# Performance work log

Measured on AMD Instinct MI355X. Metric: run time of the kernel, lower is better.

The kernel has to match this reference:

```python
import jax, jax.numpy as jnp
import numpy as np

B, N, M = 8, 1024, 1024
D_MODEL, D_HEAD, M_BITS = 1024, 128, 32
SCALE = 1.0 / np.sqrt(M_BITS)


def setup_inputs() -> dict:
    key = jax.random.key(0)
    ks = jax.random.split(key, 11)
    w_std = 1.0 / np.sqrt(D_MODEL)  # ~ nn.Linear init scale
    f32 = jnp.float32
    return {
        "Q": jax.random.normal(ks[0], (B, N, D_MODEL), dtype=f32),
        "K": jax.random.normal(ks[1], (B, M, D_MODEL), dtype=f32),
        "V": jax.random.normal(ks[2], (B, M, D_MODEL), dtype=f32),
        "Wq_boolean": jax.random.normal(ks[3], (D_MODEL, M_BITS), dtype=f32) * w_std,
        "Wk_boolean": jax.random.normal(ks[4], (D_MODEL, M_BITS), dtype=f32) * w_std,
        "Wq_tropical": jax.random.normal(ks[5], (D_MODEL, M_BITS), dtype=f32) * w_std,
        "Wk_tropical": jax.random.normal(ks[6], (D_MODEL, M_BITS), dtype=f32) * w_std,
        "Wq_real": jax.random.normal(ks[7], (D_MODEL, M_BITS), dtype=f32) * w_std,
        "Wk_real": jax.random.normal(ks[8], (D_MODEL, M_BITS), dtype=f32) * w_std,
        "Wv": jax.random.normal(ks[9], (D_MODEL, D_HEAD), dtype=f32) * w_std,
        "fusion_weights": jnp.ones((3,), dtype=f32),
        "mask": jnp.ones((B, N, M), dtype=jnp.int32),
    }


def _tropical_sim(Qe, Ke):
    # max-plus (tropical) witness similarity: sim[b,n,m] = max_d (Qe[b,n,d] + Ke[b,m,d])
    # loop over the small fixed bit dim (M_BITS=32) to avoid a [B,N,M,M_BITS] tensor
    acc = Qe[:, :, 0][:, :, None] + Ke[:, :, 0][:, None, :]
    for b in range(1, M_BITS):
        acc = jnp.maximum(acc, Qe[:, :, b][:, :, None] + Ke[:, :, b][:, None, :])
    return acc  # [B,N,M]


def reference(Q, K, V, Wq_boolean, Wk_boolean, Wq_tropical, Wk_tropical,
              Wq_real, Wk_real, Wv, fusion_weights, mask):
    # --- boolean monoid: hard-binarized codes, bit-match count ---
    Qb = (Q @ Wq_boolean > 0).astype(Q.dtype)   # [B,N,m]
    Kb = (K @ Wk_boolean > 0).astype(K.dtype)   # [B,M,m]
    sim_bool = (jnp.einsum('bnd,bmd->bnm', Qb, Kb)
                + jnp.einsum('bnd,bmd->bnm', 1.0 - Qb, 1.0 - Kb))
    # --- tropical monoid: max-plus over continuous codes ---
    sim_trop = _tropical_sim(Q @ Wq_tropical, K @ Wk_tropical)
    # --- real monoid: inner product of continuous codes ---
    sim_real = jnp.einsum('bnd,bmd->bnm', Q @ Wq_real, K @ Wk_real)
    # --- learned fusion + scaled softmax attention ---
    w = jax.nn.softmax(fusion_weights)
    scores = (w[0] * sim_bool + w[1] * sim_trop + w[2] * sim_real) * SCALE
    scores = jnp.where(mask == 0, -jnp.inf, scores)
    attn = jax.nn.softmax(scores, axis=-1)     # [B,N,M]  (dropout: eval mode, identity)
    out = jnp.einsum('bnm,bmh->bnh', attn, V @ Wv)  # [B,N,d_head]
    return out, attn
```

## Files before the change

kernel.cpp:

```cpp
#include <hip/hip_runtime.h>
#include <hip/hip_fp16.h>
#include <stdint.h>
#include <math.h>


#define SCALE_F 0.17677669529663687f

typedef float4 f4;
typedef unsigned int uint_t;
typedef unsigned short ushort_t;
typedef __attribute__((ext_vector_type(8))) short s16x8;
typedef __attribute__((ext_vector_type(8))) unsigned short u16x8;
typedef __attribute__((ext_vector_type(4))) float f32x4;

__device__ __forceinline__ ushort_t f2bf(float x) {
    unsigned u = __float_as_uint(x);
    return (ushort_t)((u + 0x7FFFu + ((u >> 16) & 1u)) >> 16);
}
__device__ __forceinline__ float bf2f(ushort_t h) {
    return __uint_as_float(((unsigned)h) << 16);
}
__device__ __forceinline__ float f4c(const f4 v, int i) {
    return i == 0 ? v.x : (i == 1 ? v.y : (i == 2 ? v.z : v.w));
}
__device__ __forceinline__ unsigned pk_add(unsigned a, unsigned b) {
    unsigned r;
    asm("v_pk_add_f16 %0, %1, %2" : "=v"(r) : "v"(a), "v"(b));
    return r;
}
__device__ __forceinline__ unsigned pk_max(unsigned a, unsigned b) {
    unsigned r;
    asm("v_pk_max_f16 %0, %1, %2" : "=v"(r) : "v"(a), "v"(b));
    return r;
}
__device__ __forceinline__ float h2f(ushort_t u) {
    __half h;
    *reinterpret_cast<ushort_t*>(&h) = u;
    return __half2float(h);
}
__device__ __forceinline__ ushort_t f2h(float x) {
    __half h = __float2half(x);
    return *reinterpret_cast<ushort_t*>(&h);
}

#define MFMA16(a, b, c) __builtin_amdgcn_mfma_f32_16x16x32_bf16((a), (b), (c), 0, 0, 0)

__device__ __forceinline__ int bo(int col, int kq) {
    return col * 64 + 8 * (kq ^ (col & 7));
}
__device__ __forceinline__ int fillk(int s) {
    return 8 * ((s & 7) ^ ((s >> 3) & 7));
}

__global__ __launch_bounds__(256)
void conv_w_kernel(const float* __restrict__ Wqb, const float* __restrict__ Wkb,
                   const float* __restrict__ Wqt, const float* __restrict__ Wkt,
                   const float* __restrict__ Wqr, const float* __restrict__ Wkr,
                   const float* __restrict__ Wv,
                   ushort_t* __restrict__ Wh, ushort_t* __restrict__ Wm,
                   ushort_t* __restrict__ Wl3,
                   ushort_t* __restrict__ Wvh, ushort_t* __restrict__ Wvm) {
    __shared__ float T[256][33];
    const int t = threadIdx.x;
    const int bid = blockIdx.x;
    const float* src;
    int kb, outRowBase, srcStride, srcColBase, side = 0;
    bool isQK, isBool;
    if (bid < 24) {
        side = bid / 12;
        int cb = (bid % 12) / 4;
        kb = bid & 3;
        const float* mats[6] = {Wqb, Wqt, Wqr, Wkb, Wkt, Wkr};
        src = mats[side * 3 + cb];
        srcStride = 32; srcColBase = 0;
        outRowBase = side * 96 + cb * 32;
        isQK = true; isBool = (cb == 0);
    } else {
        int v = bid - 24;
        int hb = v >> 2; kb = v & 3;
        src = Wv; srcStride = 128; srcColBase = hb * 32;
        outRowBase = hb * 32;
        isQK = false; isBool = false;
    }
    #pragma unroll
    for (int i = 0; i < 8; ++i) {
        int idx = t + i * 256;
        int r = idx >> 3, c4 = idx & 7;
        f4 v = *(const f4*)&src[(size_t)(kb * 256 + r) * srcStride + srcColBase + c4 * 4];
        T[r][c4 * 4 + 0] = v.x; T[r][c4 * 4 + 1] = v.y;
        T[r][c4 * 4 + 2] = v.z; T[r][c4 * 4 + 3] = v.w;
    }
    __syncthreads();
    const int col = t >> 3, kseg = t & 7;
    ushort_t* dh = isQK ? Wh : Wvh;
    ushort_t* dm = isQK ? Wm : Wvm;
    size_t obase = (size_t)(outRowBase + col) * 1024 + kb * 256 + kseg * 32;
    u16x8 ph[4], pm[4], pl[4];
    #pragma unroll
    for (int i = 0; i < 32; ++i) {
        float x = T[kseg * 32 + i][col];
        ushort_t hb_ = f2bf(x);
        float r1 = x - bf2f(hb_);
        ushort_t mb_ = f2bf(r1);
        float r2 = r1 - bf2f(mb_);
        ph[i >> 3][i & 7] = hb_;
        pm[i >> 3][i & 7] = mb_;
        pl[i >> 3][i & 7] = f2bf(r2);
    }
    #pragma unroll
    for (int i = 0; i < 4; ++i) {
        *(u16x8*)&dh[obase + i * 8] = ph[i];
        *(u16x8*)&dm[obase + i * 8] = pm[i];
    }
    if (isBool) {
        size_t lbase = (size_t)(side * 32 + col) * 1024 + kb * 256 + kseg * 32;
        #pragma unroll
        for (int i = 0; i < 4; ++i) *(u16x8*)&Wl3[lbase + i * 8] = pl[i];
    }
}


__global__ __launch_bounds__(256)
void proj_qk_kernel(const float* __restrict__ Q, const float* __restrict__ K,
                    const ushort_t* __restrict__ Wh, const ushort_t* __restrict__ Wm,
                    ushort_t* __restrict__ Qt_q, ushort_t* __restrict__ Kt_q,
                    ushort_t* __restrict__ Qrh, ushort_t* __restrict__ Qrm,
                    ushort_t* __restrict__ Krh, ushort_t* __restrict__ Krm,
                    uint_t* __restrict__ Qbits, uint_t* __restrict__ Kbits) {
    __shared__ ushort_t BH[2][6144];
    __shared__ ushort_t BM[2][4096];
    __shared__ uint_t sb[64];
    const int t = threadIdx.x, lane = t & 63, w = t >> 6;
    const int g = lane >> 4, l15 = lane & 15;
    const int side = blockIdx.x >> 7;
    const int row0 = (blockIdx.x & 127) * 64;
    const float* __restrict__ X = side ? K : Q;
    const float* __restrict__ Xrow = X + (size_t)(row0 + w * 16 + l15) * 1024;
    if (t < 64) sb[t] = 0;

    const ushort_t* srcH[3]; int dstH[3];
    #pragma unroll
    for (int i = 0; i < 3; ++i) {
        int s = t + i * 256;
        int col = s >> 3;
        srcH[i] = Wh + (size_t)(side * 96 + col) * 1024 + fillk(s);
        dstH[i] = s * 8;
    }
    const ushort_t* srcM[2]; int dstM[2];
    #pragma unroll
    for (int i = 0; i < 2; ++i) {
        int s = t + i * 256;
        int col = s >> 3;
        int f = (col < 32) ? col : col + 32;
        srcM[i] = Wm + (size_t)(side * 96 + f) * 1024 + fillk(s);
        dstM[i] = s * 8;
    }

    f32x4 accB[2], accT[2], accR[2];
    #pragma unroll
    for (int i = 0; i < 2; ++i) {
        accB[i] = f32x4{0.f, 0.f, 0.f, 0.f};
        accT[i] = f32x4{0.f, 0.f, 0.f, 0.f};
        accR[i] = f32x4{0.f, 0.f, 0.f, 0.f};
    }

    f4 arE[4], arO[4];
    u16x8 hE[3], mE[2], hO[3], mO[2];

    auto STAGE_A = [&](int k0, f4* ar) {
        ar[0] = *(const f4*)&Xrow[k0 + g * 8];
        ar[1] = *(const f4*)&Xrow[k0 + g * 8 + 4];
        ar[2] = *(const f4*)&Xrow[k0 + 32 + g * 8];
        ar[3] = *(const f4*)&Xrow[k0 + 32 + g * 8 + 4];
    };
    auto STAGE_B = [&](int k0, u16x8* hh, u16x8* mm) {
        #pragma unroll
        for (int i = 0; i < 3; ++i) hh[i] = *(const u16x8*)(srcH[i] + k0);
        #pragma unroll
        for (int i = 0; i < 2; ++i) mm[i] = *(const u16x8*)(srcM[i] + k0);
    };
    auto WRITE_B = [&](int buf, u16x8* hh, u16x8* mm) {
        #pragma unroll
        for (int i = 0; i < 3; ++i) *(u16x8*)&BH[buf][dstH[i]] = hh[i];
        #pragma unroll
        for (int i = 0; i < 2; ++i) *(u16x8*)&BM[buf][dstM[i]] = mm[i];
    };
    auto COMPUTE = [&](int buf, f4* ar) {
        #pragma unroll
        for (int ks = 0; ks < 2; ++ks) {
            u16x8 ah, am, al;
            #pragma unroll
            for (int j = 0; j < 8; ++j) {
                float x = (j < 4) ? f4c(ar[2 * ks], j) : f4c(ar[2 * ks + 1], j - 4);
                ushort_t hb_ = f2bf(x);
                float r1 = x - bf2f(hb_);
                ushort_t mb_ = f2bf(r1);
                ah[j] = hb_; am[j] = mb_;
                al[j] = f2bf(r1 - bf2f(mb_));
            }
            s16x8 a1 = (s16x8)ah, a2 = (s16x8)am, a3 = (s16x8)al;
            const int kq = ks * 4 + g;
            #pragma unroll
            for (int cf = 0; cf < 2; ++cf) {
                int col = cf * 16 + l15;
                s16x8 bh = *(const s16x8*)&BH[buf][bo(col, kq)];
                s16x8 bm = *(const s16x8*)&BM[buf][bo(col, kq)];
                accB[cf] = MFMA16(a1, bh, accB[cf]);
                accB[cf] = MFMA16(a1, bm, accB[cf]);
                accB[cf] = MFMA16(a2, bh, accB[cf]);
                accB[cf] = MFMA16(a2, bm, accB[cf]);
                accB[cf] = MFMA16(a3, bh, accB[cf]);
            }
            #pragma unroll
            for (int cf = 0; cf < 2; ++cf) {
                int col = 32 + cf * 16 + l15;
                s16x8 bh = *(const s16x8*)&BH[buf][bo(col, kq)];
                accT[cf] = MFMA16(a1, bh, accT[cf]);
            }
            #pragma unroll
            for (int cf = 0; cf < 2; ++cf) {
                int colh = 64 + cf * 16 + l15;
                int colm = 32 + cf * 16 + l15;
                s16x8 bh = *(const s16x8*)&BH[buf][bo(colh, kq)];
                s16x8 bm = *(const s16x8*)&BM[buf][bo(colm, kq)];
                accR[cf] = MFMA16(a1, bh, accR[cf]);
                accR[cf] = MFMA16(a1, bm, accR[cf]);
                accR[cf] = MFMA16(a2, bh, accR[cf]);
            }
        }
    };

    STAGE_A(0, arE);
    STAGE_B(0, hE, mE);
    WRITE_B(0, hE, mE);
    __syncthreads();

    for (int cc = 0; cc < 8; ++cc) {
        const int kE = cc * 128;
        STAGE_A(kE + 64, arO);
        STAGE_B(kE + 64, hO, mO);
        COMPUTE(0, arE);
        WRITE_B(1, hO, mO);
        __syncthreads();
        if (cc < 7) {
            STAGE_A(kE + 128, arE);
            STAGE_B(kE + 128, hE, mE);
        }
        COMPUTE(1, arO);
        if (cc < 7) WRITE_B(0, hE, mE);
        __syncthreads();
    }

    #pragma unroll
    for (int cf = 0; cf < 2; ++cf)
        #pragma unroll
        for (int r = 0; r < 4; ++r) {
            unsigned long long bm = __ballot(accB[cf][r] > 0.f);
            if (lane == 0) {
                #pragma unroll
                for (int gg = 0; gg < 4; ++gg)
                    sb[w * 16 + gg * 4 + r] |=
                        (uint_t)((bm >> (16 * gg)) & 0xFFFFull) << (16 * cf);
            }
        }
    ushort_t* Tt = side ? Kt_q : Qt_q;
    ushort_t* Rh = side ? Krh : Qrh;
    ushort_t* Rm = side ? Krm : Qrm;
    #pragma unroll
    for (int cf = 0; cf < 2; ++cf)
        #pragma unroll
        for (int r = 0; r < 4; ++r) {
            int grow = row0 + w * 16 + g * 4 + r;
            Tt[(size_t)grow * 32 + cf * 16 + l15] = f2h(accT[cf][r]);
            float v = accR[cf][r];
            ushort_t h = f2bf(v);
            Rh[(size_t)grow * 32 + cf * 16 + l15] = h;
            Rm[(size_t)grow * 32 + cf * 16 + l15] = f2bf(v - bf2f(h));
        }
    __syncthreads();
    uint_t* Tb = side ? Kbits : Qbits;
    if (t < 64) Tb[row0 + t] = sb[t];
}


__global__ __launch_bounds__(256)
void proj_v_kernel(const float* __restrict__ V,
                   const ushort_t* __restrict__ Wvh, const ushort_t* __restrict__ Wvm,
                   ushort_t* __restrict__ VphT, ushort_t* __restrict__ VpmT) {
    __shared__ ushort_t VH[2][8192], VM[2][8192];
    const int t = threadIdx.x, lane = t & 63, w = t >> 6;
    const int g = lane >> 4, l15 = lane & 15;
    const int tile = blockIdx.x;
    const int row0 = tile * 32;
    const int rowh = (w & 1) * 16, hbase = (w >> 1) * 64;
    const float* __restrict__ Xrow = V + (size_t)(row0 + rowh + l15) * 1024;

    const ushort_t* srcH[4]; const ushort_t* srcM[4]; int dst[4];
    #pragma unroll
    for (int i = 0; i < 4; ++i) {
        int s = t + i * 256;
        int col = s >> 3;
        srcH[i] = Wvh + (size_t)col * 1024 + fillk(s);
        srcM[i] = Wvm + (size_t)col * 1024 + fillk(s);
        dst[i] = s * 8;
    }

    f32x4 acc[4];
    #pragma unroll
    for (int i = 0; i < 4; ++i) acc[i] = f32x4{0.f, 0.f, 0.f, 0.f};

    f4 arE[4], arO[4];
    u16x8 hE[4], mE[4], hO[4], mO[4];

    auto STAGE_A = [&](int k0, f4* ar) {
        ar[0] = *(const f4*)&Xrow[k0 + g * 8];
        ar[1] = *(const f4*)&Xrow[k0 + g * 8 + 4];
        ar[2] = *(const f4*)&Xrow[k0 + 32 + g * 8];
        ar[3] = *(const f4*)&Xrow[k0 + 32 + g * 8 + 4];
    };
    auto STAGE_B = [&](int k0, u16x8* hh, u16x8* mm) {
        #pragma unroll
        for (int i = 0; i < 4; ++i) {
            hh[i] = *(const u16x8*)(srcH[i] + k0);
            mm[i] = *(const u16x8*)(srcM[i] + k0);
        }
    };
    auto WRITE_B = [&](int buf, u16x8* hh, u16x8* mm) {
        #pragma unroll
        for (int i = 0; i < 4; ++i) {
            *(u16x8*)&VH[buf][dst[i]] = hh[i];
            *(u16x8*)&VM[buf][dst[i]] = mm[i];
        }
    };
    auto COMPUTE = [&](int buf, f4* ar) {
        #pragma unroll
        for (int ks = 0; ks < 2; ++ks) {
            u16x8 ah, am;
            #pragma unroll
            for (int j = 0; j < 8; ++j) {
                float x = (j < 4) ? f4c(ar[2 * ks], j) : f4c(ar[2 * ks + 1], j - 4);
                ushort_t hb_ = f2bf(x);
                ah[j] = hb_; am[j] = f2bf(x - bf2f(hb_));
            }
            s16x8 a1 = (s16x8)ah, a2 = (s16x8)am;
            const int kq = ks * 4 + g;
            #pragma unroll
            for (int cf = 0; cf < 4; ++cf) {
                int col = hbase + cf * 16 + l15;
                s16x8 bh = *(const s16x8*)&VH[buf][bo(col, kq)];
                s16x8 bm = *(const s16x8*)&VM[buf][bo(col, kq)];
                acc[cf] = MFMA16(a1, bh, acc[cf]);
                acc[cf] = MFMA16(a1, bm, acc[cf]);
                acc[cf] = MFMA16(a2, bh, acc[cf]);
            }
        }
    };

    STAGE_A(0, arE);
    STAGE_B(0, hE, mE);
    WRITE_B(0, hE, mE);
    __syncthreads();
    for (int cc = 0; cc < 8; ++cc) {
        const int kE = cc * 128;
        STAGE_A(kE + 64, arO);
        STAGE_B(kE + 64, hO, mO);
        COMPUTE(0, arE);
        WRITE_B(1, hO, mO);
        __syncthreads();
        if (cc < 7) {
            STAGE_A(kE + 128, arE);
            STAGE_B(kE + 128, hE, mE);
        }
        COMPUTE(1, arO);
        if (cc < 7) WRITE_B(0, hE, mE);
        __syncthreads();
    }

    const int b = tile >> 5;
    const int mbase = (tile & 31) * 32 + rowh + g * 4;
    #pragma unroll
    for (int cf = 0; cf < 4; ++cf) {
        int colh = hbase + cf * 16 + l15;
        float v0 = acc[cf][0], v1 = acc[cf][1], v2 = acc[cf][2], v3 = acc[cf][3];
        ushort_t h0 = f2bf(v0), h1 = f2bf(v1), h2_ = f2bf(v2), h3 = f2bf(v3);
        ushort4 hv = make_ushort4(h0, h1, h2_, h3);
        ushort4 mv = make_ushort4(f2bf(v0 - bf2f(h0)), f2bf(v1 - bf2f(h1)),
                                  f2bf(v2 - bf2f(h2_)), f2bf(v3 - bf2f(h3)));
        size_t ob = (size_t)(b * 128 + colh) * 1024 + mbase;
        *(ushort4*)&VphT[ob] = hv;
        *(ushort4*)&VpmT[ob] = mv;
    }
}


__global__ __launch_bounds__(256)
void scores_kernel(const ushort_t* __restrict__ Qt_q, const ushort_t* __restrict__ Kt_q,
                   const ushort_t* __restrict__ Qrh, const ushort_t* __restrict__ Qrm,
                   const ushort_t* __restrict__ Krh, const ushort_t* __restrict__ Krm,
                   const uint_t* __restrict__ Qbits, const uint_t* __restrict__ Kbits,
                   const float* __restrict__ fw, float* __restrict__ attn) {
    __shared__ uint_t KtT[4][1024][4];
    const int t = threadIdx.x, lane = t & 63, w = t >> 6;
    const int g = lane >> 4, l15 = lane & 15;
    const int b = blockIdx.y, n0 = blockIdx.x * 16;
    const int rowA = b * 1024 + n0;

    #pragma unroll
    for (int i = 0; i < 16; ++i) {
        int j4 = i >> 2, row = t + (i & 3) * 256;
        u16x8 v = *(const u16x8*)&Kt_q[(size_t)(b * 1024 + row) * 32 + j4 * 8];
        *(u16x8*)&KtT[j4][row][0] = v;
    }

    s16x8 qrh = *(const s16x8*)&Qrh[(size_t)(rowA + l15) * 32 + g * 8];
    s16x8 qrm = *(const s16x8*)&Qrm[(size_t)(rowA + l15) * 32 + g * 8];
    uint_t qt[4][16], qb[4];
    #pragma unroll
    for (int r = 0; r < 4; ++r) {
        const uint_t* p = (const uint_t*)&Qt_q[(size_t)(rowA + 4 * g + r) * 32];
        #pragma unroll
        for (int j = 0; j < 16; ++j) qt[r][j] = p[j];
        qb[r] = Qbits[rowA + 4 * g + r];
    }
    const float f0 = fw[0], f1 = fw[1], f2 = fw[2];
    const float fm = fmaxf(f0, fmaxf(f1, f2));
    const float e0 = __expf(f0 - fm), e1 = __expf(f1 - fm), e2 = __expf(f2 - fm);
    const float wi = 1.f / (e0 + e1 + e2);
    const float w0 = e0 * wi, w1 = e1 * wi, w2 = e2 * wi;
    __syncthreads();

    for (int i = 0; i < 16; ++i) {
        const int m0 = (w + 4 * i) * 16;
        const int mrow = b * 1024 + m0;
        s16x8 krh = *(const s16x8*)&Krh[(size_t)(mrow + l15) * 32 + g * 8];
        s16x8 krm = *(const s16x8*)&Krm[(size_t)(mrow + l15) * 32 + g * 8];
        uint_t kb = Kbits[mrow + l15];

        f32x4 rc = f32x4{0.f, 0.f, 0.f, 0.f};
        rc = MFMA16(qrh, krh, rc);
        rc = MFMA16(qrh, krm, rc);
        rc = MFMA16(qrm, krh, rc);

        const int m = m0 + l15;
        uint_t kk[16];
        uint4 k0v = *(const uint4*)&KtT[0][m][0];
        uint4 k1v = *(const uint4*)&KtT[1][m][0];
        uint4 k2v = *(const uint4*)&KtT[2][m][0];
        uint4 k3v = *(const uint4*)&KtT[3][m][0];
        kk[0] = k0v.x; kk[1] = k0v.y; kk[2] = k0v.z; kk[3] = k0v.w;
        kk[4] = k1v.x; kk[5] = k1v.y; kk[6] = k1v.z; kk[7] = k1v.w;
        kk[8] = k2v.x; kk[9] = k2v.y; kk[10] = k2v.z; kk[11] = k2v.w;
        kk[12] = k3v.x; kk[13] = k3v.y; kk[14] = k3v.z; kk[15] = k3v.w;

        float trop[4];
        #pragma unroll
        for (int r = 0; r < 4; ++r) {
            unsigned a = pk_add(qt[r][0], kk[0]);
            #pragma unroll
            for (int j = 1; j < 16; ++j)
                a = pk_max(a, pk_add(qt[r][j], kk[j]));
            trop[r] = fmaxf(h2f((ushort_t)(a & 0xFFFF)), h2f((ushort_t)(a >> 16)));
        }
        #pragma unroll
        for (int r = 0; r < 4; ++r) {
            float cnt = (float)(32 - __popc(qb[r] ^ kb));
            attn[(size_t)(rowA + 4 * g + r) * 1024 + m] =
                (w0 * cnt + w1 * trop[r] + w2 * rc[r]) * SCALE_F;
        }
    }
}


__global__ __launch_bounds__(256)
void softmax_kernel(float* __restrict__ attn, const int* __restrict__ mask) {
    const int row = blockIdx.x;
    const int t = threadIdx.x;
    const f4  s4 = ((const f4*)attn)[(size_t)row * 256 + t];
    const int4 m4 = ((const int4*)mask)[(size_t)row * 256 + t];
    const float v0 = m4.x ? s4.x : -INFINITY;
    const float v1 = m4.y ? s4.y : -INFINITY;
    const float v2 = m4.z ? s4.z : -INFINITY;
    const float v3 = m4.w ? s4.w : -INFINITY;

    float tm = fmaxf(fmaxf(v0, v1), fmaxf(v2, v3));
    #pragma unroll
    for (int off = 32; off >= 1; off >>= 1) tm = fmaxf(tm, __shfl_xor(tm, off, 64));
    __shared__ float rmax[4], rsum[4];
    if ((t & 63) == 0) rmax[t >> 6] = tm;
    __syncthreads();
    const float gm = fmaxf(fmaxf(rmax[0], rmax[1]), fmaxf(rmax[2], rmax[3]));

    const float x0 = m4.x ? __expf(v0 - gm) : 0.f;
    const float x1 = m4.y ? __expf(v1 - gm) : 0.f;
    const float x2 = m4.z ? __expf(v2 - gm) : 0.f;
    const float x3 = m4.w ? __expf(v3 - gm) : 0.f;
    float ts = (x0 + x1) + (x2 + x3);
    #pragma unroll
    for (int off = 32; off >= 1; off >>= 1) ts += __shfl_xor(ts, off, 64);
    if ((t & 63) == 0) rsum[t >> 6] = ts;
    __syncthreads();
    const float inv = 1.f / ((rsum[0] + rsum[1]) + (rsum[2] + rsum[3]));

    ((f4*)attn)[(size_t)row * 256 + t] = make_float4(x0 * inv, x1 * inv, x2 * inv, x3 * inv);
}


__global__ __launch_bounds__(256)
void pv_kernel(const float* __restrict__ attn,
               const ushort_t* __restrict__ VphT, const ushort_t* __restrict__ VpmT,
               float* __restrict__ out) {
    __shared__ ushort_t VH[2][8192], VM[2][8192];
    const int t = threadIdx.x, lane = t & 63, w = t >> 6;
    const int g = lane >> 4, l15 = lane & 15;
    const int b = blockIdx.x >> 5;
    const int n0 = (blockIdx.x & 31) * 32;
    const int rowh = (w & 1) * 16, hbase = (w >> 1) * 64;
    const float* __restrict__ Arow = attn + (size_t)(b * 1024 + n0 + rowh + l15) * 1024;

    const ushort_t* srcH[4]; const ushort_t* srcM[4]; int dst[4];
    #pragma unroll
    for (int i = 0; i < 4; ++i) {
        int s = t + i * 256;
        int col = s >> 3;
        srcH[i] = VphT + (size_t)(b * 128 + col) * 1024 + fillk(s);
        srcM[i] = VpmT + (size_t)(b * 128 + col) * 1024 + fillk(s);
        dst[i] = s * 8;
    }

    f32x4 acc[4];
    #pragma unroll
    for (int i = 0; i < 4; ++i) acc[i] = f32x4{0.f, 0.f, 0.f, 0.f};

    f4 arE[4], arO[4];
    u16x8 hE[4], mE[4], hO[4], mO[4];

    auto STAGE_A = [&](int k0, f4* ar) {
        ar[0] = *(const f4*)&Arow[k0 + g * 8];
        ar[1] = *(const f4*)&Arow[k0 + g * 8 + 4];
        ar[2] = *(const f4*)&Arow[k0 + 32 + g * 8];
        ar[3] = *(const f4*)&Arow[k0 + 32 + g * 8 + 4];
    };
    auto STAGE_B = [&](int k0, u16x8* hh, u16x8* mm) {
        #pragma unroll
        for (int i = 0; i < 4; ++i) {
            hh[i] = *(const u16x8*)(srcH[i] + k0);
            mm[i] = *(const u16x8*)(srcM[i] + k0);
        }
    };
    auto WRITE_B = [&](int buf, u16x8* hh, u16x8* mm) {
        #pragma unroll
        for (int i = 0; i < 4; ++i) {
            *(u16x8*)&VH[buf][dst[i]] = hh[i];
            *(u16x8*)&VM[buf][dst[i]] = mm[i];
        }
    };
    auto COMPUTE = [&](int buf, f4* ar) {
        #pragma unroll
        for (int ks = 0; ks < 2; ++ks) {
            u16x8 ah, am;
            #pragma unroll
            for (int j = 0; j < 8; ++j) {
                float x = (j < 4) ? f4c(ar[2 * ks], j) : f4c(ar[2 * ks + 1], j - 4);
                ushort_t hb_ = f2bf(x);
                ah[j] = hb_; am[j] = f2bf(x - bf2f(hb_));
            }
            s16x8 a1 = (s16x8)ah, a2 = (s16x8)am;
            const int kq = ks * 4 + g;
            #pragma unroll
            for (int cf = 0; cf < 4; ++cf) {
                int col = hbase + cf * 16 + l15;
                s16x8 bh = *(const s16x8*)&VH[buf][bo(col, kq)];
                s16x8 bm = *(const s16x8*)&VM[buf][bo(col, kq)];
                acc[cf] = MFMA16(a1, bh, acc[cf]);
                acc[cf] = MFMA16(a1, bm, acc[cf]);
                acc[cf] = MFMA16(a2, bh, acc[cf]);
            }
        }
    };

    STAGE_A(0, arE);
    STAGE_B(0, hE, mE);
    WRITE_B(0, hE, mE);
    __syncthreads();
    for (int cc = 0; cc < 8; ++cc) {
        const int kE = cc * 128;
        STAGE_A(kE + 64, arO);
        STAGE_B(kE + 64, hO, mO);
        COMPUTE(0, arE);
        WRITE_B(1, hO, mO);
        __syncthreads();
        if (cc < 7) {
            STAGE_A(kE + 128, arE);
            STAGE_B(kE + 128, hE, mE);
        }
        COMPUTE(1, arO);
        if (cc < 7) WRITE_B(0, hE, mE);
        __syncthreads();
    }

    #pragma unroll
    for (int cf = 0; cf < 4; ++cf)
        #pragma unroll
        for (int r = 0; r < 4; ++r)
            out[(size_t)(b * 1024 + n0 + rowh + g * 4 + r) * 128 + hbase + cf * 16 + l15] =
                acc[cf][r];
}


extern "C" void kernel_launch(void* const* d_in, const int* in_sizes, int n_in,
                              void* d_out, int out_size, void* d_ws, size_t ws_size,
                              hipStream_t stream) {
    const float* Q   = (const float*)d_in[0];
    const float* K   = (const float*)d_in[1];
    const float* V   = (const float*)d_in[2];
    const float* Wqb = (const float*)d_in[3];
    const float* Wkb = (const float*)d_in[4];
    const float* Wqt = (const float*)d_in[5];
    const float* Wkt = (const float*)d_in[6];
    const float* Wqr = (const float*)d_in[7];
    const float* Wkr = (const float*)d_in[8];
    const float* Wv  = (const float*)d_in[9];
    const float* fw  = (const float*)d_in[10];
    const int*  mask = (const int*)d_in[11];

    ushort_t* wsu = (ushort_t*)d_ws;
    ushort_t* Wh   = wsu;
    ushort_t* Wm   = Wh + 196608;
    ushort_t* Wl3  = Wm + 196608;
    ushort_t* Wvh  = Wl3 + 65536;
    ushort_t* Wvm  = Wvh + 131072;
    ushort_t* Qt_q = Wvm + 131072;
    ushort_t* Kt_q = Qt_q + 262144;
    ushort_t* Qrh  = Kt_q + 262144;
    ushort_t* Qrm  = Qrh + 262144;
    ushort_t* Krh  = Qrm + 262144;
    ushort_t* Krm  = Krh + 262144;
    ushort_t* VphT = Krm + 262144;
    ushort_t* VpmT = VphT + 1048576;
    uint_t* Qbits = (uint_t*)(VpmT + 1048576);
    uint_t* Kbits = Qbits + 8192;

    float* out  = (float*)d_out;
    float* attn = out + 1048576;

    conv_w_kernel<<<40, 256, 0, stream>>>(Wqb, Wkb, Wqt, Wkt, Wqr, Wkr, Wv,
                                          Wh, Wm, Wl3, Wvh, Wvm);
    proj_qk_kernel<<<256, 256, 0, stream>>>(Q, K, Wh, Wm,
                                            Qt_q, Kt_q, Qrh, Qrm, Krh, Krm, Qbits, Kbits);
    proj_v_kernel<<<256, 256, 0, stream>>>(V, Wvh, Wvm, VphT, VpmT);
    scores_kernel<<<dim3(64, 8), 256, 0, stream>>>(Qt_q, Kt_q, Qrh, Qrm, Krh, Krm,
                                                   Qbits, Kbits, fw, attn);
    softmax_kernel<<<8192, 256, 0, stream>>>(attn, mask);
    pv_kernel<<<256, 256, 0, stream>>>(attn, VphT, VpmT, out);
}
```

Baseline: 268.5 us.

## Fuse scores, softmax and PV into one attention kernel; split projection work

Replaces the separate scores, softmax and PV kernels with one fused kernel. It keeps a 16-row score tile in shared memory, applies the mask, does the softmax there, writes attn once, and packs the probabilities as hi/lo bf16 for the PV MFMAs. This removes the extra round trips of the 32 MB attn matrix through global memory (write scores, read and rewrite in softmax, read in PV). The QK and V projection kernels are also re-tiled to twice as many, smaller blocks, and in the QK kernel waves now specialise on either the boolean codes or the tropical/real codes. The cost is fewer rows per block in the fused kernel and K tiles read directly from global memory instead of staged in LDS.

```diff
diff --git a/kernel.cpp b/kernel.cpp
--- a/kernel.cpp
+++ b/kernel.cpp
@@ -129,14 +129,17 @@
                     uint_t* __restrict__ Qbits, uint_t* __restrict__ Kbits) {
     __shared__ ushort_t BH[2][6144];
     __shared__ ushort_t BM[2][4096];
-    __shared__ uint_t sb[64];
+    __shared__ uint_t sb[32];
     const int t = threadIdx.x, lane = t & 63, w = t >> 6;
     const int g = lane >> 4, l15 = lane & 15;
-    const int side = blockIdx.x >> 7;
-    const int row0 = (blockIdx.x & 127) * 64;
+    const int side = blockIdx.x >> 8;
+    const int tile = blockIdx.x & 255;
+    const int row0 = tile * 32;
+    const int rg = w >> 1;
+    const int ch = w & 1;
     const float* __restrict__ X = side ? K : Q;
-    const float* __restrict__ Xrow = X + (size_t)(row0 + w * 16 + l15) * 1024;
-    if (t < 64) sb[t] = 0;
+    const float* __restrict__ Xrow = X + (size_t)(row0 + rg * 16 + l15) * 1024;
+    if (t < 32) sb[t] = 0;
 
     const ushort_t* srcH[3]; int dstH[3];
     #pragma unroll
@@ -198,34 +201,38 @@
                 ah[j] = hb_; am[j] = mb_;
                 al[j] = f2bf(r1 - bf2f(mb_));
             }
-            s16x8 a1 = (s16x8)ah, a2 = (s16x8)am, a3 = (s16x8)al;
+            s16x8 a1 = (s16x8)ah, a2 = (s16x8)am;
             const int kq = ks * 4 + g;
-            #pragma unroll
-            for (int cf = 0; cf < 2; ++cf) {
-                int col = cf * 16 + l15;
-                s16x8 bh = *(const s16x8*)&BH[buf][bo(col, kq)];
-                s16x8 bm = *(const s16x8*)&BM[buf][bo(col, kq)];
-                accB[cf] = MFMA16(a1, bh, accB[cf]);
-                accB[cf] = MFMA16(a1, bm, accB[cf]);
-                accB[cf] = MFMA16(a2, bh, accB[cf]);
-                accB[cf] = MFMA16(a2, bm, accB[cf]);
-                accB[cf] = MFMA16(a3, bh, accB[cf]);
-            }
-            #pragma unroll
-            for (int cf = 0; cf < 2; ++cf) {
-                int col = 32 + cf * 16 + l15;
-                s16x8 bh = *(const s16x8*)&BH[buf][bo(col, kq)];
-                accT[cf] = MFMA16(a1, bh, accT[cf]);
-            }
-            #pragma unroll
-            for (int cf = 0; cf < 2; ++cf) {
-                int colh = 64 + cf * 16 + l15;
-                int colm = 32 + cf * 16 + l15;
-                s16x8 bh = *(const s16x8*)&BH[buf][bo(colh, kq)];
-                s16x8 bm = *(const s16x8*)&BM[buf][bo(colm, kq)];
-                accR[cf] = MFMA16(a1, bh, accR[cf]);
-                accR[cf] = MFMA16(a1, bm, accR[cf]);
-                accR[cf] = MFMA16(a2, bh, accR[cf]);
+            if (ch == 0) {
+                s16x8 a3 = (s16x8)al;
+                #pragma unroll
+                for (int cf = 0; cf < 2; ++cf) {
+                    int col = cf * 16 + l15;
+                    s16x8 bh = *(const s16x8*)&BH[buf][bo(col, kq)];
+                    s16x8 bm = *(const s16x8*)&BM[buf][bo(col, kq)];
+                    accB[cf] = MFMA16(a1, bh, accB[cf]);
+                    accB[cf] = MFMA16(a1, bm, accB[cf]);
+                    accB[cf] = MFMA16(a2, bh, accB[cf]);
+                    accB[cf] = MFMA16(a2, bm, accB[cf]);
+                    accB[cf] = MFMA16(a3, bh, accB[cf]);
+                }
+            } else {
+                #pragma unroll
+                for (int cf = 0; cf < 2; ++cf) {
+                    int col = 32 + cf * 16 + l15;
+                    s16x8 bh = *(const s16x8*)&BH[buf][bo(col, kq)];
+                    accT[cf] = MFMA16(a1, bh, accT[cf]);
+                }
+                #pragma unroll
+                for (int cf = 0; cf < 2; ++cf) {
+                    int colh = 64 + cf * 16 + l15;
+                    int colm = 32 + cf * 16 + l15;
+                    s16x8 bh = *(const s16x8*)&BH[buf][bo(colh, kq)];
+                    s16x8 bm = *(const s16x8*)&BM[buf][bo(colm, kq)];
+                    accR[cf] = MFMA16(a1, bh, accR[cf]);
+                    accR[cf] = MFMA16(a1, bm, accR[cf]);
+                    accR[cf] = MFMA16(a2, bh, accR[cf]);
+                }
             }
         }
     };
@@ -234,7 +241,6 @@
     STAGE_B(0, hE, mE);
     WRITE_B(0, hE, mE);
     __syncthreads();
-
     for (int cc = 0; cc < 8; ++cc) {
         const int kE = cc * 128;
         STAGE_A(kE + 64, arO);
@@ -251,35 +257,38 @@
         __syncthreads();
     }
 
-    #pragma unroll
-    for (int cf = 0; cf < 2; ++cf)
-        #pragma unroll
-        for (int r = 0; r < 4; ++r) {
-            unsigned long long bm = __ballot(accB[cf][r] > 0.f);
-            if (lane == 0) {
-                #pragma unroll
-                for (int gg = 0; gg < 4; ++gg)
-                    sb[w * 16 + gg * 4 + r] |=
-                        (uint_t)((bm >> (16 * gg)) & 0xFFFFull) << (16 * cf);
+    if (ch == 0) {
+        #pragma unroll
+        for (int cf = 0; cf < 2; ++cf)
+            #pragma unroll
+            for (int r = 0; r < 4; ++r) {
+                unsigned long long bm = __ballot(accB[cf][r] > 0.f);
+                if (lane == 0) {
+                    #pragma unroll
+                    for (int gg = 0; gg < 4; ++gg)
+                        sb[rg * 16 + gg * 4 + r] |=
+                            (uint_t)((bm >> (16 * gg)) & 0xFFFFull) << (16 * cf);
+                }
             }
-        }
-    ushort_t* Tt = side ? Kt_q : Qt_q;
-    ushort_t* Rh = side ? Krh : Qrh;
-    ushort_t* Rm = side ? Krm : Qrm;
-    #pragma unroll
-    for (int cf = 0; cf < 2; ++cf)
-        #pragma unroll
-        for (int r = 0; r < 4; ++r) {
-            int grow = row0 + w * 16 + g * 4 + r;
-            Tt[(size_t)grow * 32 + cf * 16 + l15] = f2h(accT[cf][r]);
-            float v = accR[cf][r];
-            ushort_t h = f2bf(v);
-            Rh[(size_t)grow * 32 + cf * 16 + l15] = h;
-            Rm[(size_t)grow * 32 + cf * 16 + l15] = f2bf(v - bf2f(h));
-        }
+    } else {
+        ushort_t* Tt = side ? Kt_q : Qt_q;
+        ushort_t* Rh = side ? Krh : Qrh;
+        ushort_t* Rm = side ? Krm : Qrm;
+        #pragma unroll
+        for (int cf = 0; cf < 2; ++cf)
+            #pragma unroll
+            for (int r = 0; r < 4; ++r) {
+                int grow = row0 + rg * 16 + g * 4 + r;
+                Tt[(size_t)grow * 32 + cf * 16 + l15] = f2h(accT[cf][r]);
+                float v = accR[cf][r];
+                ushort_t h = f2bf(v);
+                Rh[(size_t)grow * 32 + cf * 16 + l15] = h;
+                Rm[(size_t)grow * 32 + cf * 16 + l15] = f2bf(v - bf2f(h));
+            }
+    }
     __syncthreads();
     uint_t* Tb = side ? Kbits : Qbits;
-    if (t < 64) Tb[row0 + t] = sb[t];
+    if (t < 32) Tb[row0 + t] = sb[t];
 }
 
 
@@ -291,9 +300,9 @@
     const int t = threadIdx.x, lane = t & 63, w = t >> 6;
     const int g = lane >> 4, l15 = lane & 15;
     const int tile = blockIdx.x;
-    const int row0 = tile * 32;
-    const int rowh = (w & 1) * 16, hbase = (w >> 1) * 64;
-    const float* __restrict__ Xrow = V + (size_t)(row0 + rowh + l15) * 1024;
+    const int row0 = tile * 16;
+    const int hbase = w * 32;
+    const float* __restrict__ Xrow = V + (size_t)(row0 + l15) * 1024;
 
     const ushort_t* srcH[4]; const ushort_t* srcM[4]; int dst[4];
     #pragma unroll
@@ -305,9 +314,9 @@
         dst[i] = s * 8;
     }
 
-    f32x4 acc[4];
-    #pragma unroll
-    for (int i = 0; i < 4; ++i) acc[i] = f32x4{0.f, 0.f, 0.f, 0.f};
+    f32x4 acc[2];
+    acc[0] = f32x4{0.f, 0.f, 0.f, 0.f};
+    acc[1] = f32x4{0.f, 0.f, 0.f, 0.f};
 
     f4 arE[4], arO[4];
     u16x8 hE[4], mE[4], hO[4], mO[4];
@@ -345,7 +354,7 @@
             s16x8 a1 = (s16x8)ah, a2 = (s16x8)am;
             const int kq = ks * 4 + g;
             #pragma unroll
-            for (int cf = 0; cf < 4; ++cf) {
+            for (int cf = 0; cf < 2; ++cf) {
                 int col = hbase + cf * 16 + l15;
                 s16x8 bh = *(const s16x8*)&VH[buf][bo(col, kq)];
                 s16x8 bm = *(const s16x8*)&VM[buf][bo(col, kq)];
@@ -376,41 +385,40 @@
         __syncthreads();
     }
 
-    const int b = tile >> 5;
-    const int mbase = (tile & 31) * 32 + rowh + g * 4;
-    #pragma unroll
-    for (int cf = 0; cf < 4; ++cf) {
+    const int b = tile >> 6;
+    const int mb = (tile & 63) * 16 + g * 4;
+    #pragma unroll
+    for (int cf = 0; cf < 2; ++cf) {
         int colh = hbase + cf * 16 + l15;
         float v0 = acc[cf][0], v1 = acc[cf][1], v2 = acc[cf][2], v3 = acc[cf][3];
         ushort_t h0 = f2bf(v0), h1 = f2bf(v1), h2_ = f2bf(v2), h3 = f2bf(v3);
         ushort4 hv = make_ushort4(h0, h1, h2_, h3);
         ushort4 mv = make_ushort4(f2bf(v0 - bf2f(h0)), f2bf(v1 - bf2f(h1)),
                                   f2bf(v2 - bf2f(h2_)), f2bf(v3 - bf2f(h3)));
-        size_t ob = (size_t)(b * 128 + colh) * 1024 + mbase;
+        size_t ob = (size_t)(b * 128 + colh) * 1024 + mb;
         *(ushort4*)&VphT[ob] = hv;
         *(ushort4*)&VpmT[ob] = mv;
     }
 }
 
 
+#define SW 1036
+
 __global__ __launch_bounds__(256)
-void scores_kernel(const ushort_t* __restrict__ Qt_q, const ushort_t* __restrict__ Kt_q,
-                   const ushort_t* __restrict__ Qrh, const ushort_t* __restrict__ Qrm,
-                   const ushort_t* __restrict__ Krh, const ushort_t* __restrict__ Krm,
-                   const uint_t* __restrict__ Qbits, const uint_t* __restrict__ Kbits,
-                   const float* __restrict__ fw, float* __restrict__ attn) {
-    __shared__ uint_t KtT[4][1024][4];
+void fused_attn_kernel(const ushort_t* __restrict__ Qt_q, const ushort_t* __restrict__ Kt_q,
+                       const ushort_t* __restrict__ Qrh, const ushort_t* __restrict__ Qrm,
+                       const ushort_t* __restrict__ Krh, const ushort_t* __restrict__ Krm,
+                       const uint_t* __restrict__ Qbits, const uint_t* __restrict__ Kbits,
+                       const ushort_t* __restrict__ VphT, const ushort_t* __restrict__ VpmT,
+                       const int* __restrict__ mask, const float* __restrict__ fw,
+                       float* __restrict__ attn, float* __restrict__ out) {
+    __shared__ uint_t S[16][SW];
+    __shared__ float rmaxS[16], rinvS[16];
     const int t = threadIdx.x, lane = t & 63, w = t >> 6;
     const int g = lane >> 4, l15 = lane & 15;
-    const int b = blockIdx.y, n0 = blockIdx.x * 16;
+    const int bid = blockIdx.x;
+    const int b = bid & 7, n0 = (bid >> 3) * 16;
     const int rowA = b * 1024 + n0;
-
-    #pragma unroll
-    for (int i = 0; i < 16; ++i) {
-        int j4 = i >> 2, row = t + (i & 3) * 256;
-        u16x8 v = *(const u16x8*)&Kt_q[(size_t)(b * 1024 + row) * 32 + j4 * 8];
-        *(u16x8*)&KtT[j4][row][0] = v;
-    }
 
     s16x8 qrh = *(const s16x8*)&Qrh[(size_t)(rowA + l15) * 32 + g * 8];
     s16x8 qrm = *(const s16x8*)&Qrm[(size_t)(rowA + l15) * 32 + g * 8];
@@ -427,30 +435,32 @@
     const float e0 = __expf(f0 - fm), e1 = __expf(f1 - fm), e2 = __expf(f2 - fm);
     const float wi = 1.f / (e0 + e1 + e2);
     const float w0 = e0 * wi, w1 = e1 * wi, w2 = e2 * wi;
-    __syncthreads();
 
     for (int i = 0; i < 16; ++i) {
         const int m0 = (w + 4 * i) * 16;
         const int mrow = b * 1024 + m0;
+        const uint_t* ktp = (const uint_t*)&Kt_q[(size_t)(mrow + l15) * 32];
+        uint_t kk[16];
+        uint4 k0v = *(const uint4*)&ktp[0];
+        uint4 k1v = *(const uint4*)&ktp[4];
+        uint4 k2v = *(const uint4*)&ktp[8];
+        uint4 k3v = *(const uint4*)&ktp[12];
+        kk[0] = k0v.x; kk[1] = k0v.y; kk[2] = k0v.z; kk[3] = k0v.w;
+        kk[4] = k1v.x; kk[5] = k1v.y; kk[6] = k1v.z; kk[7] = k1v.w;
+        kk[8] = k2v.x; kk[9] = k2v.y; kk[10] = k2v.z; kk[11] = k2v.w;
+        kk[12] = k3v.x; kk[13] = k3v.y; kk[14] = k3v.z; kk[15] = k3v.w;
         s16x8 krh = *(const s16x8*)&Krh[(size_t)(mrow + l15) * 32 + g * 8];
         s16x8 krm = *(const s16x8*)&Krm[(size_t)(mrow + l15) * 32 + g * 8];
         uint_t kb = Kbits[mrow + l15];
+        int mk[4];
+        #pragma unroll
+        for (int r = 0; r < 4; ++r)
+            mk[r] = mask[(size_t)(rowA + 4 * g + r) * 1024 + m0 + l15];
 
         f32x4 rc = f32x4{0.f, 0.f, 0.f, 0.f};
         rc = MFMA16(qrh, krh, rc);
         rc = MFMA16(qrh, krm, rc);
         rc = MFMA16(qrm, krh, rc);
-
-        const int m = m0 + l15;
-        uint_t kk[16];
-        uint4 k0v = *(const uint4*)&KtT[0][m][0];
-        uint4 k1v = *(const uint4*)&KtT[1][m][0];
-        uint4 k2v = *(const uint4*)&KtT[2][m][0];
-        uint4 k3v = *(const uint4*)&KtT[3][m][0];
-        kk[0] = k0v.x; kk[1] = k0v.y; kk[2] = k0v.z; kk[3] = k0v.w;
-        kk[4] = k1v.x; kk[5] = k1v.y; kk[6] = k1v.z; kk[7] = k1v.w;
-        kk[8] = k2v.x; kk[9] = k2v.y; kk[10] = k2v.z; kk[11] = k2v.w;
-        kk[12] = k3v.x; kk[13] = k3v.y; kk[14] = k3v.z; kk[15] = k3v.w;
 
         float trop[4];
         #pragma unroll
@@ -464,146 +474,81 @@
         #pragma unroll
         for (int r = 0; r < 4; ++r) {
             float cnt = (float)(32 - __popc(qb[r] ^ kb));
-            attn[(size_t)(rowA + 4 * g + r) * 1024 + m] =
-                (w0 * cnt + w1 * trop[r] + w2 * rc[r]) * SCALE_F;
-        }
-    }
-}
-
-
-__global__ __launch_bounds__(256)
-void softmax_kernel(float* __restrict__ attn, const int* __restrict__ mask) {
-    const int row = blockIdx.x;
-    const int t = threadIdx.x;
-    const f4  s4 = ((const f4*)attn)[(size_t)row * 256 + t];
-    const int4 m4 = ((const int4*)mask)[(size_t)row * 256 + t];
-    const float v0 = m4.x ? s4.x : -INFINITY;
-    const float v1 = m4.y ? s4.y : -INFINITY;
-    const float v2 = m4.z ? s4.z : -INFINITY;
-    const float v3 = m4.w ? s4.w : -INFINITY;
-
-    float tm = fmaxf(fmaxf(v0, v1), fmaxf(v2, v3));
-    #pragma unroll
-    for (int off = 32; off >= 1; off >>= 1) tm = fmaxf(tm, __shfl_xor(tm, off, 64));
-    __shared__ float rmax[4], rsum[4];
-    if ((t & 63) == 0) rmax[t >> 6] = tm;
-    __syncthreads();
-    const float gm = fmaxf(fmaxf(rmax[0], rmax[1]), fmaxf(rmax[2], rmax[3]));
-
-    const float x0 = m4.x ? __expf(v0 - gm) : 0.f;
-    const float x1 = m4.y ? __expf(v1 - gm) : 0.f;
-    const float x2 = m4.z ? __expf(v2 - gm) : 0.f;
-    const float x3 = m4.w ? __expf(v3 - gm) : 0.f;
-    float ts = (x0 + x1) + (x2 + x3);
-    #pragma unroll
-    for (int off = 32; off >= 1; off >>= 1) ts += __shfl_xor(ts, off, 64);
-    if ((t & 63) == 0) rsum[t >> 6] = ts;
-    __syncthreads();
-    const float inv = 1.f / ((rsum[0] + rsum[1]) + (rsum[2] + rsum[3]));
-
-    ((f4*)attn)[(size_t)row * 256 + t] = make_float4(x0 * inv, x1 * inv, x2 * inv, x3 * inv);
-}
-
-
-__global__ __launch_bounds__(256)
-void pv_kernel(const float* __restrict__ attn,
-               const ushort_t* __restrict__ VphT, const ushort_t* __restrict__ VpmT,
-               float* __restrict__ out) {
-    __shared__ ushort_t VH[2][8192], VM[2][8192];
-    const int t = threadIdx.x, lane = t & 63, w = t >> 6;
-    const int g = lane >> 4, l15 = lane & 15;
-    const int b = blockIdx.x >> 5;
-    const int n0 = (blockIdx.x & 31) * 32;
-    const int rowh = (w & 1) * 16, hbase = (w >> 1) * 64;
-    const float* __restrict__ Arow = attn + (size_t)(b * 1024 + n0 + rowh + l15) * 1024;
-
-    const ushort_t* srcH[4]; const ushort_t* srcM[4]; int dst[4];
-    #pragma unroll
-    for (int i = 0; i < 4; ++i) {
-        int s = t + i * 256;
-        int col = s >> 3;
-        srcH[i] = VphT + (size_t)(b * 128 + col) * 1024 + fillk(s);
-        srcM[i] = VpmT + (size_t)(b * 128 + col) * 1024 + fillk(s);
-        dst[i] = s * 8;
-    }
-
-    f32x4 acc[4];
-    #pragma unroll
-    for (int i = 0; i < 4; ++i) acc[i] = f32x4{0.f, 0.f, 0.f, 0.f};
-
-    f4 arE[4], arO[4];
-    u16x8 hE[4], mE[4], hO[4], mO[4];
-
-    auto STAGE_A = [&](int k0, f4* ar) {
-        ar[0] = *(const f4*)&Arow[k0 + g * 8];
-        ar[1] = *(const f4*)&Arow[k0 + g * 8 + 4];
-        ar[2] = *(const f4*)&Arow[k0 + 32 + g * 8];
-        ar[3] = *(const f4*)&Arow[k0 + 32 + g * 8 + 4];
-    };
-    auto STAGE_B = [&](int k0, u16x8* hh, u16x8* mm) {
-        #pragma unroll
-        for (int i = 0; i < 4; ++i) {
-            hh[i] = *(const u16x8*)(srcH[i] + k0);
-            mm[i] = *(const u16x8*)(srcM[i] + k0);
-        }
-    };
-    auto WRITE_B = [&](int buf, u16x8* hh, u16x8* mm) {
-        #pragma unroll
-        for (int i = 0; i < 4; ++i) {
-            *(u16x8*)&VH[buf][dst[i]] = hh[i];
-            *(u16x8*)&VM[buf][dst[i]] = mm[i];
-        }
-    };
-    auto COMPUTE = [&](int buf, f4* ar) {
-        #pragma unroll
-        for (int ks = 0; ks < 2; ++ks) {
-            u16x8 ah, am;
-            #pragma unroll
-            for (int j = 0; j < 8; ++j) {
-                float x = (j < 4) ? f4c(ar[2 * ks], j) : f4c(ar[2 * ks + 1], j - 4);
-                ushort_t hb_ = f2bf(x);
-                ah[j] = hb_; am[j] = f2bf(x - bf2f(hb_));
-            }
-            s16x8 a1 = (s16x8)ah, a2 = (s16x8)am;
-            const int kq = ks * 4 + g;
-            #pragma unroll
-            for (int cf = 0; cf < 4; ++cf) {
-                int col = hbase + cf * 16 + l15;
-                s16x8 bh = *(const s16x8*)&VH[buf][bo(col, kq)];
-                s16x8 bm = *(const s16x8*)&VM[buf][bo(col, kq)];
-                acc[cf] = MFMA16(a1, bh, acc[cf]);
-                acc[cf] = MFMA16(a1, bm, acc[cf]);
-                acc[cf] = MFMA16(a2, bh, acc[cf]);
-            }
-        }
-    };
-
-    STAGE_A(0, arE);
-    STAGE_B(0, hE, mE);
-    WRITE_B(0, hE, mE);
-    __syncthreads();
-    for (int cc = 0; cc < 8; ++cc) {
-        const int kE = cc * 128;
-        STAGE_A(kE + 64, arO);
-        STAGE_B(kE + 64, hO, mO);
-        COMPUTE(0, arE);
-        WRITE_B(1, hO, mO);
-        __syncthreads();
-        if (cc < 7) {
-            STAGE_A(kE + 128, arE);
-            STAGE_B(kE + 128, hE, mE);
-        }
-        COMPUTE(1, arO);
-        if (cc < 7) WRITE_B(0, hE, mE);
-        __syncthreads();
-    }
-
-    #pragma unroll
-    for (int cf = 0; cf < 4; ++cf)
+            float s = (w0 * cnt + w1 * trop[r] + w2 * rc[r]) * SCALE_F;
+            *(float*)&S[4 * g + r][m0 + l15] = mk[r] ? s : -INFINITY;
+        }
+    }
+    __syncthreads();
+
+    #pragma unroll
+    for (int q = 0; q < 4; ++q) {
+        const int row = 4 * w + q;
+        float mx = -INFINITY;
+        #pragma unroll
+        for (int j = 0; j < 16; ++j)
+            mx = fmaxf(mx, *(const float*)&S[row][lane + j * 64]);
+        #pragma unroll
+        for (int off = 32; off >= 1; off >>= 1) mx = fmaxf(mx, __shfl_xor(mx, off, 64));
+        float sm = 0.f;
+        #pragma unroll
+        for (int j = 0; j < 16; ++j)
+            sm += __expf(*(const float*)&S[row][lane + j * 64] - mx);
+        #pragma unroll
+        for (int off = 32; off >= 1; off >>= 1) sm += __shfl_xor(sm, off, 64);
+        if (lane == 0) { rmaxS[row] = mx; rinvS[row] = 1.f / sm; }
+    }
+    __syncthreads();
+
+    #pragma unroll
+    for (int j = 0; j < 16; ++j) {
+        const float mx = rmaxS[j], inv = rinvS[j];
+        f4 s4 = *(const f4*)&S[j][t * 4];
+        float p0 = __expf(s4.x - mx) * inv;
+        float p1 = __expf(s4.y - mx) * inv;
+        float p2 = __expf(s4.z - mx) * inv;
+        float p3 = __expf(s4.w - mx) * inv;
+        *(f4*)&attn[(size_t)(rowA + j) * 1024 + t * 4] = make_float4(p0, p1, p2, p3);
+        ushort_t h0 = f2bf(p0), h1 = f2bf(p1), h2_ = f2bf(p2), h3 = f2bf(p3);
+        uint4 pk;
+        pk.x = (uint_t)h0 | ((uint_t)f2bf(p0 - bf2f(h0)) << 16);
+        pk.y = (uint_t)h1 | ((uint_t)f2bf(p1 - bf2f(h1)) << 16);
+        pk.z = (uint_t)h2_ | ((uint_t)f2bf(p2 - bf2f(h2_)) << 16);
+        pk.w = (uint_t)h3 | ((uint_t)f2bf(p3 - bf2f(h3)) << 16);
+        *(uint4*)&S[j][t * 4] = pk;
+    }
+    __syncthreads();
+
+    const int hbase = w * 32;
+    f32x4 acc[2];
+    acc[0] = f32x4{0.f, 0.f, 0.f, 0.f};
+    acc[1] = f32x4{0.f, 0.f, 0.f, 0.f};
+    for (int mc = 0; mc < 32; ++mc) {
+        const int m0 = mc * 32;
+        uint4 ua = *(const uint4*)&S[l15][m0 + g * 8];
+        uint4 ub = *(const uint4*)&S[l15][m0 + g * 8 + 4];
+        u16x8 a1v, a2v;
+        uint_t uu[8] = {ua.x, ua.y, ua.z, ua.w, ub.x, ub.y, ub.z, ub.w};
+        #pragma unroll
+        for (int j = 0; j < 8; ++j) {
+            a1v[j] = (ushort_t)(uu[j] & 0xFFFFu);
+            a2v[j] = (ushort_t)(uu[j] >> 16);
+        }
+        s16x8 a1 = (s16x8)a1v, a2 = (s16x8)a2v;
+        #pragma unroll
+        for (int cf = 0; cf < 2; ++cf) {
+            const size_t vb = (size_t)(b * 128 + hbase + cf * 16 + l15) * 1024 + m0 + g * 8;
+            s16x8 bh = *(const s16x8*)&VphT[vb];
+            s16x8 bm = *(const s16x8*)&VpmT[vb];
+            acc[cf] = MFMA16(a1, bh, acc[cf]);
+            acc[cf] = MFMA16(a1, bm, acc[cf]);
+            acc[cf] = MFMA16(a2, bh, acc[cf]);
+        }
+    }
+    #pragma unroll
+    for (int cf = 0; cf < 2; ++cf)
         #pragma unroll
         for (int r = 0; r < 4; ++r)
-            out[(size_t)(b * 1024 + n0 + rowh + g * 4 + r) * 128 + hbase + cf * 16 + l15] =
-                acc[cf][r];
+            out[(size_t)(rowA + 4 * g + r) * 128 + hbase + cf * 16 + l15] = acc[cf][r];
 }
 
 
@@ -645,11 +590,10 @@
 
     conv_w_kernel<<<40, 256, 0, stream>>>(Wqb, Wkb, Wqt, Wkt, Wqr, Wkr, Wv,
                                           Wh, Wm, Wl3, Wvh, Wvm);
-    proj_qk_kernel<<<256, 256, 0, stream>>>(Q, K, Wh, Wm,
+    proj_qk_kernel<<<512, 256, 0, stream>>>(Q, K, Wh, Wm,
                                             Qt_q, Kt_q, Qrh, Qrm, Krh, Krm, Qbits, Kbits);
-    proj_v_kernel<<<256, 256, 0, stream>>>(V, Wvh, Wvm, VphT, VpmT);
-    scores_kernel<<<dim3(64, 8), 256, 0, stream>>>(Qt_q, Kt_q, Qrh, Qrm, Krh, Krm,
-                                                   Qbits, Kbits, fw, attn);
-    softmax_kernel<<<8192, 256, 0, stream>>>(attn, mask);
-    pv_kernel<<<256, 256, 0, stream>>>(attn, VphT, VpmT, out);
-}
+    proj_v_kernel<<<512, 256, 0, stream>>>(V, Wvh, Wvm, VphT, VpmT);
+    fused_attn_kernel<<<512, 256, 0, stream>>>(Qt_q, Kt_q, Qrh, Qrm, Krh, Krm,
+                                               Qbits, Kbits, VphT, VpmT,
+                                               mask, fw, attn, out);
+}
```

New measurement: 267.8 us. No clear change (-0.3%).
